# Kernel optimization log

Measured on AMD Instinct MI355X. Metric: run time of the kernel, lower is better.

The kernel has to match this reference:

```python
import jax, jax.numpy as jnp
import numpy as np

N = 50000
E = 600000
IN_DIM = 128
HID = 128
TIME_EMB = 32
T_STEPS = 100


def setup_inputs() -> dict:
    key = jax.random.key(0)
    ks = jax.random.split(key, 24)
    def lin_w(k, fi, fo):
        return (jax.random.normal(k, (fi, fo), jnp.float32) / np.sqrt(fi)).astype(jnp.float32)
    inp = {
        "target_features": jax.random.normal(ks[0], (N, IN_DIM), jnp.float32),
        "edge_index_v1": jax.random.randint(ks[1], (2, E), 0, N),
        "edge_index_v2": jax.random.randint(ks[2], (2, E), 0, N),
        "t": 57,
        "noise_v1": jax.random.normal(ks[3], (N, HID), jnp.float32),
        "noise_v2": jax.random.normal(ks[4], (N, HID), jnp.float32),
        # encoder GCN weights
        "enc_W1": lin_w(ks[5], IN_DIM, HID), "enc_b1": jnp.zeros((HID,), jnp.float32),
        "enc_W2": lin_w(ks[6], HID, HID),    "enc_b2": jnp.zeros((HID,), jnp.float32),
        # denoiser time MLP
        "tm_W1": lin_w(ks[7], 1, TIME_EMB),       "tm_b1": jnp.zeros((TIME_EMB,), jnp.float32),
        "tm_W2": lin_w(ks[8], TIME_EMB, HID),     "tm_b2": jnp.zeros((HID,), jnp.float32),
        # denoiser GCNs
        "g1_W": lin_w(ks[9], 3 * HID, HID), "g1_b": jnp.zeros((HID,), jnp.float32),
        "g2_W": lin_w(ks[10], HID, HID),    "g2_b": jnp.zeros((HID,), jnp.float32),
        "g3_W": lin_w(ks[11], HID, HID),    "g3_b": jnp.zeros((HID,), jnp.float32),
    }
    return inp


def _gcn_norm(edge_index, n):
    # add self-loops, symmetric normalization (PyG GCNConv default)
    loops = jnp.arange(n)
    src = jnp.concatenate([edge_index[0], loops])
    dst = jnp.concatenate([edge_index[1], loops])
    deg = jax.ops.segment_sum(jnp.ones_like(dst, dtype=jnp.float32), dst, num_segments=n)
    dinv = jnp.where(deg > 0, jax.lax.rsqrt(deg), 0.0)
    norm = dinv[src] * dinv[dst]  # (E+N,)
    return src, dst, norm


def _gcn(x, W, b, src, dst, norm, n):
    h = x @ W                                    # (N, out)
    msg = h[src] * norm[:, None]                 # gather + scale
    return jax.ops.segment_sum(msg, dst, num_segments=n) + b  # scatter-add


def reference(target_features, edge_index_v1, edge_index_v2, t, noise_v1, noise_v2,
              enc_W1, enc_b1, enc_W2, enc_b2,
              tm_W1, tm_b1, tm_W2, tm_b2,
              g1_W, g1_b, g2_W, g2_b, g3_W, g3_b):
    n = target_features.shape[0]
    e1 = _gcn_norm(edge_index_v1, n)
    e2 = _gcn_norm(edge_index_v2, n)

    def encoder(x, ed):
        h = jax.nn.relu(_gcn(x, enc_W1, enc_b1, *ed, n))
        return _gcn(h, enc_W2, enc_b2, *ed, n)

    h0_v1 = encoder(target_features, e1)
    h0_v2 = encoder(target_features, e2)

    # linear beta schedule coefficients at timestep t
    betas = jnp.linspace(1e-4, 0.02, T_STEPS)
    alpha_bars = jnp.cumprod(1.0 - betas)
    sqrt_ab = jnp.sqrt(alpha_bars)[t]
    sqrt_1m = jnp.sqrt(1.0 - alpha_bars)[t]

    h_t_v1 = sqrt_ab * h0_v1 + sqrt_1m * noise_v1
    h_t_v2 = sqrt_ab * h0_v2 + sqrt_1m * noise_v2

    # time embedding (same scalar t expanded to all nodes)
    t_float = jnp.full((n, 1), t, jnp.float32)
    t_emb = jax.nn.silu(t_float @ tm_W1 + tm_b1) @ tm_W2 + tm_b2  # (N, HID)

    def denoiser(h_self, h_other, ed):
        h = jnp.concatenate([h_self, h_other, t_emb], axis=-1)  # (N, 3*HID)
        h = jax.nn.relu(_gcn(h, g1_W, g1_b, *ed, n))
        h = jax.nn.relu(_gcn(h, g2_W, g2_b, *ed, n))
        return _gcn(h, g3_W, g3_b, *ed, n)

    pred_v1 = denoiser(h_t_v1, h_t_v2, e1)
    pred_v2 = denoiser(h_t_v2, h_t_v1, e2)

    L_diff = jnp.mean((pred_v1 - noise_v1) ** 2) + jnp.mean((pred_v2 - noise_v2) ** 2)
    h_diff = 0.5 * (h0_v1 + h0_v2)
    return h_diff, L_diff
```

## Files before the change

### kernel.cpp

```cpp
#include <hip/hip_runtime.h>

#define NN 50000
#define NE 600000

typedef __attribute__((ext_vector_type(8))) short short8;
typedef __attribute__((ext_vector_type(4))) float f32x4;

static inline int divup(int a, int b) { return (a + b - 1) / b; }

__device__ inline unsigned short f2bf(float f) {
    unsigned int u = __float_as_uint(f);
    unsigned int r = (u + 0x7FFFu + ((u >> 16) & 1u)) >> 16;
    return (unsigned short)r;
}
__device__ inline float bflo(unsigned int u) { return __uint_as_float(u << 16); }
__device__ inline float bfhi(unsigned int u) { return __uint_as_float(u & 0xFFFF0000u); }


__global__ void k_zero_int(int* p, int n) {
    int i = blockIdx.x * blockDim.x + threadIdx.x;
    int stride = gridDim.x * blockDim.x;
    for (; i < n; i += stride) p[i] = 0;
}

__global__ void k_scalars(const int* __restrict__ t_p,
                          const float* __restrict__ tmW1, const float* __restrict__ tmb1,
                          const float* __restrict__ tmW2, const float* __restrict__ tmb2,
                          const float* __restrict__ g1W,
                          float* __restrict__ scal, float* __restrict__ lout) {
    __shared__ float e32[32];
    __shared__ float temb[128];
    const int tid = threadIdx.x;
    const int t = t_p[0];
    if (tid < 32) {
        float x = (float)t * tmW1[tid] + tmb1[tid];
        e32[tid] = x / (1.0f + expf(-x));
    }
    __syncthreads();
    float acc = tmb2[tid];
    for (int j = 0; j < 32; ++j) acc += e32[j] * tmW2[j * 128 + tid];
    temb[tid] = acc;
    __syncthreads();
    float cv = 0.0f;
    for (int j = 0; j < 128; ++j) cv += temb[j] * g1W[(256 + j) * 128 + tid];
    scal[2 + tid] = cv;
    if (tid == 0) {
        double ab = 1.0;
        for (int i = 0; i <= t; ++i) {
            double beta = 1e-4 + (0.02 - 1e-4) * (double)i / 99.0;
            ab *= (1.0 - beta);
        }
        scal[0] = (float)sqrt(ab);
        scal[1] = (float)sqrt(1.0 - ab);
        lout[0] = 0.0f;
    }
}

__global__ void k_wprep(const float* __restrict__ encW1, const float* __restrict__ encW2,
                        const float* __restrict__ g1W, const float* __restrict__ g2W,
                        const float* __restrict__ g3W, unsigned short* __restrict__ WtS) {
    int i = blockIdx.x * blockDim.x + threadIdx.x;
    if (i >= 6 * 16384) return;
    int m = i >> 14;
    int r = i & 16383;
    int k = r >> 7;
    int n = r & 127;
    const float* src;
    switch (m) {
        case 0: src = encW1; break;
        case 1: src = encW2; break;
        case 2: src = g1W; break;
        case 3: src = g1W + 16384; break;
        case 4: src = g2W; break;
        default: src = g3W; break;
    }
    unsigned short v = f2bf(src[k * 128 + n]);
    unsigned int byte = (((unsigned)n << 8) | ((unsigned)k << 1)) ^ (((unsigned)n & 7u) << 4);
    WtS[(m << 14) + (byte >> 1)] = v;
}

__global__ void k_xcast(const float* __restrict__ in, unsigned short* __restrict__ out, int n4) {
    int i = blockIdx.x * blockDim.x + threadIdx.x;
    int stride = gridDim.x * blockDim.x;
    for (; i < n4; i += stride) {
        float4 v = ((const float4*)in)[i];
        ushort4 o;
        o.x = f2bf(v.x); o.y = f2bf(v.y); o.z = f2bf(v.z); o.w = f2bf(v.w);
        ((ushort4*)out)[i] = o;
    }
}

__global__ void k_hist(const int* __restrict__ dst, int* __restrict__ cnt, int e) {
    int i = blockIdx.x * blockDim.x + threadIdx.x;
    if (i < e) atomicAdd(&cnt[dst[i]], 1);
}

#define SCAN_B 256
__global__ void k_scan1(const int* __restrict__ cnt, int* __restrict__ exc,
                        int* __restrict__ bsum, int n) {
    __shared__ int s[SCAN_B];
    int i = blockIdx.x * SCAN_B + threadIdx.x;
    int v = (i < n) ? cnt[i] : 0;
    s[threadIdx.x] = v;
    __syncthreads();
    for (int off = 1; off < SCAN_B; off <<= 1) {
        int tv = (threadIdx.x >= off) ? s[threadIdx.x - off] : 0;
        __syncthreads();
        s[threadIdx.x] += tv;
        __syncthreads();
    }
    if (i < n) exc[i] = s[threadIdx.x] - v;
    if (threadIdx.x == SCAN_B - 1) bsum[blockIdx.x] = s[SCAN_B - 1];
}

__global__ void k_scan2(int* __restrict__ bsum, int nb) {
    __shared__ int s[SCAN_B];
    int v = (threadIdx.x < nb) ? bsum[threadIdx.x] : 0;
    s[threadIdx.x] = v;
    __syncthreads();
    for (int off = 1; off < SCAN_B; off <<= 1) {
        int tv = (threadIdx.x >= off) ? s[threadIdx.x - off] : 0;
        __syncthreads();
        s[threadIdx.x] += tv;
        __syncthreads();
    }
    if (threadIdx.x < nb) bsum[threadIdx.x] = s[threadIdx.x] - v;
}

__global__ void k_scan3(int* __restrict__ exc, const int* __restrict__ bsum, int n, int total) {
    int i = blockIdx.x * SCAN_B + threadIdx.x;
    if (i < n) exc[i] += bsum[blockIdx.x];
    if (i == 0) exc[n] = total;
}

__global__ void k_fill(const int* __restrict__ src, const int* __restrict__ dst,
                       const int* __restrict__ rowptr, int* __restrict__ fill,
                       int* __restrict__ colA, int e) {
    int i = blockIdx.x * blockDim.x + threadIdx.x;
    if (i < e) {
        int d = dst[i];
        int p = atomicAdd(&fill[d], 1);
        colA[rowptr[d] + p] = src[i];
    }
}

__global__ void k_dinv(const int* __restrict__ cnt, float* __restrict__ dinv, int n) {
    int i = blockIdx.x * blockDim.x + threadIdx.x;
    if (i < n) dinv[i] = rsqrtf((float)cnt[i] + 1.0f);
}

__global__ __launch_bounds__(256) void k_mgemm(
    const unsigned short* __restrict__ A, const unsigned short* __restrict__ Wa,
    const unsigned short* __restrict__ B, const unsigned short* __restrict__ Wb,
    const float* __restrict__ cvec, unsigned short* __restrict__ out, int nrows) {
    __shared__ unsigned short sW[16384];
    const int tid = threadIdx.x;
    const int wv = tid >> 6;
    const int l = tid & 63;
    const int lrow = l & 15;
    const int lk = l >> 4;
    const int r0 = blockIdx.x * 64 + wv * 16;

    f32x4 acc[8];
#pragma unroll
    for (int ct = 0; ct < 8; ++ct) acc[ct] = (f32x4){0.f, 0.f, 0.f, 0.f};

    const unsigned short* Aptr[2] = {A, B};
    const unsigned short* Wptr[2] = {Wa, Wb};
    const int np = (B != nullptr) ? 2 : 1;

    int arow = r0 + lrow;
    if (arow >= nrows) arow = nrows - 1;

    for (int p = 0; p < np; ++p) {
        __syncthreads();
        {
            const uint4* s = (const uint4*)Wptr[p];
            uint4* d = (uint4*)sW;
#pragma unroll
            for (int j = 0; j < 8; ++j) d[tid + j * 256] = s[tid + j * 256];
        }
        __syncthreads();
        const unsigned short* abase = Aptr[p] + (size_t)arow * 128 + lk * 8;
#pragma unroll
        for (int ks = 0; ks < 4; ++ks) {
            short8 af = *(const short8*)(abase + ks * 32);
            const int kb2 = (lk * 8 + ks * 32) << 1;
#pragma unroll
            for (int ct = 0; ct < 8; ++ct) {
                int n = ct * 16 + lrow;
                int byteoff = ((n << 8) + kb2) ^ ((l & 7) << 4);
                short8 bf = *(const short8*)((const char*)sW + byteoff);
                acc[ct] = __builtin_amdgcn_mfma_f32_16x16x32_bf16(af, bf, acc[ct], 0, 0, 0);
            }
        }
    }
#pragma unroll
    for (int ct = 0; ct < 8; ++ct) {
        float cv = cvec ? cvec[ct * 16 + lrow] : 0.0f;
#pragma unroll
        for (int rg = 0; rg < 4; ++rg) {
            int row = r0 + lk * 4 + rg;
            if (row < nrows) out[(size_t)row * 128 + ct * 16 + lrow] = f2bf(acc[ct][rg] + cv);
        }
    }
}

__global__ __launch_bounds__(256) void k_agg(
    const unsigned short* __restrict__ h, const int* __restrict__ rowptr,
    const int* __restrict__ colA, const float* __restrict__ dinv,
    const float* __restrict__ bias, unsigned short* __restrict__ out, int n, int do_relu) {
    const int d = (blockIdx.x * blockDim.x + threadIdx.x) >> 6;
    const int l = threadIdx.x & 63;
    if (d >= n) return;
    const int lg = l >> 4;
    const int ll = l & 15;
    const float di = dinv[d];

    float acc[8];
#pragma unroll
    for (int k = 0; k < 8; ++k) acc[k] = 0.0f;

    const int e0 = rowptr[d];
    const int e1 = rowptr[d + 1];
    for (int base = e0; base < e1; base += 64) {
        int cnt = min(64, e1 - base);
        int cs = 0;
        float ws = 0.0f;
        if (base + l < e1) {
            cs = colA[base + l];
            ws = dinv[cs];
        }
        for (int j4 = 0; j4 < cnt; j4 += 4) {
            int idx = j4 + lg;
            int s = __shfl(cs, idx);
            float w = __shfl(ws, idx);
            uint4 u = *((const uint4*)(h + (size_t)s * 128) + ll);
            acc[0] += w * bflo(u.x);
            acc[1] += w * bfhi(u.x);
            acc[2] += w * bflo(u.y);
            acc[3] += w * bfhi(u.y);
            acc[4] += w * bflo(u.z);
            acc[5] += w * bfhi(u.z);
            acc[6] += w * bflo(u.w);
            acc[7] += w * bfhi(u.w);
        }
    }
#pragma unroll
    for (int k = 0; k < 8; ++k) {
        acc[k] += __shfl_xor(acc[k], 16);
        acc[k] += __shfl_xor(acc[k], 32);
    }
    if (lg == 0) {
        uint4 su = *((const uint4*)(h + (size_t)d * 128) + ll);
        float4 b0 = ((const float4*)bias)[ll * 2];
        float4 b1 = ((const float4*)bias)[ll * 2 + 1];
        float sf[8] = {bflo(su.x), bfhi(su.x), bflo(su.y), bfhi(su.y),
                       bflo(su.z), bfhi(su.z), bflo(su.w), bfhi(su.w)};
        float bb[8] = {b0.x, b0.y, b0.z, b0.w, b1.x, b1.y, b1.z, b1.w};
        unsigned short o[8];
#pragma unroll
        for (int k = 0; k < 8; ++k) {
            float v = di * (acc[k] + di * sf[k]) + bb[k];
            if (do_relu) v = fmaxf(v, 0.0f);
            o[k] = f2bf(v);
        }
        uint4 ov;
        ov.x = (unsigned int)o[0] | ((unsigned int)o[1] << 16);
        ov.y = (unsigned int)o[2] | ((unsigned int)o[3] << 16);
        ov.z = (unsigned int)o[4] | ((unsigned int)o[5] << 16);
        ov.w = (unsigned int)o[6] | ((unsigned int)o[7] << 16);
        *((uint4*)(out + (size_t)d * 128) + ll) = ov;
    }
}

__global__ void k_mix(const unsigned short* __restrict__ F1, const unsigned short* __restrict__ F2,
                      const float* __restrict__ n1, const float* __restrict__ n2,
                      const float* __restrict__ scal, float* __restrict__ hdiff,
                      unsigned short* __restrict__ B1, unsigned short* __restrict__ B2, int total2) {
    const float sa = scal[0];
    const float sm = scal[1];
    int i = blockIdx.x * blockDim.x + threadIdx.x;
    const int stride = gridDim.x * blockDim.x;
    for (; i < total2; i += stride) {
        unsigned int u1 = ((const unsigned int*)F1)[i];
        unsigned int u2 = ((const unsigned int*)F2)[i];
        float a0 = bflo(u1), a1 = bfhi(u1);
        float b0 = bflo(u2), b1 = bfhi(u2);
        float2 x = ((const float2*)n1)[i];
        float2 y = ((const float2*)n2)[i];
        float2 hd;
        hd.x = 0.5f * (a0 + b0);
        hd.y = 0.5f * (a1 + b1);
        ((float2*)hdiff)[i] = hd;
        float h1x = sa * a0 + sm * x.x, h1y = sa * a1 + sm * x.y;
        float h2x = sa * b0 + sm * y.x, h2y = sa * b1 + sm * y.y;
        ((unsigned int*)B1)[i] = (unsigned int)f2bf(h1x) | ((unsigned int)f2bf(h1y) << 16);
        ((unsigned int*)B2)[i] = (unsigned int)f2bf(h2x) | ((unsigned int)f2bf(h2y) << 16);
    }
}

__global__ void k_loss(const unsigned short* __restrict__ P1, const unsigned short* __restrict__ P2,
                       const float* __restrict__ n1, const float* __restrict__ n2,
                       float* __restrict__ outs, int total2, float inv_total) {
    float s = 0.0f;
    int i = blockIdx.x * blockDim.x + threadIdx.x;
    const int stride = gridDim.x * blockDim.x;
    for (; i < total2; i += stride) {
        unsigned int u1 = ((const unsigned int*)P1)[i];
        unsigned int u2 = ((const unsigned int*)P2)[i];
        float2 x = ((const float2*)n1)[i];
        float2 y = ((const float2*)n2)[i];
        float d0 = bflo(u1) - x.x, d1 = bfhi(u1) - x.y;
        float d2 = bflo(u2) - y.x, d3 = bfhi(u2) - y.y;
        s += d0 * d0 + d1 * d1 + d2 * d2 + d3 * d3;
    }
    __shared__ float red[4];
    for (int off = 32; off > 0; off >>= 1) s += __shfl_down(s, off, 64);
    const int lane = threadIdx.x & 63;
    const int wid = threadIdx.x >> 6;
    if (lane == 0) red[wid] = s;
    __syncthreads();
    if (threadIdx.x == 0) {
        float t = red[0] + red[1] + red[2] + red[3];
        atomicAdd(outs, t * inv_total);
    }
}

extern "C" void kernel_launch(void* const* d_in, const int* in_sizes, int n_in,
                              void* d_out, int out_size, void* d_ws, size_t ws_size,
                              hipStream_t stream) {
    const float* X      = (const float*)d_in[0];
    const int*   ei1    = (const int*)d_in[1];
    const int*   ei2    = (const int*)d_in[2];
    const int*   t_p    = (const int*)d_in[3];
    const float* noise1 = (const float*)d_in[4];
    const float* noise2 = (const float*)d_in[5];
    const float* encW1  = (const float*)d_in[6];
    const float* encb1  = (const float*)d_in[7];
    const float* encW2  = (const float*)d_in[8];
    const float* encb2  = (const float*)d_in[9];
    const float* tmW1   = (const float*)d_in[10];
    const float* tmb1   = (const float*)d_in[11];
    const float* tmW2   = (const float*)d_in[12];
    const float* tmb2   = (const float*)d_in[13];
    const float* g1W    = (const float*)d_in[14];
    const float* g1b    = (const float*)d_in[15];
    const float* g2W    = (const float*)d_in[16];
    const float* g2b    = (const float*)d_in[17];
    const float* g3W    = (const float*)d_in[18];
    const float* g3b    = (const float*)d_in[19];

    float* out_hdiff = (float*)d_out;
    float* out_L     = (float*)d_out + (size_t)NN * 128;

    char* p = (char*)d_ws;
    auto alloc = [&](size_t bytes) -> void* {
        void* r = (void*)p;
        p += (bytes + 255) & ~(size_t)255;
        return r;
    };
    int* cnts = (int*)alloc((size_t)4 * NN * sizeof(int));
    int *cnt1 = cnts, *cnt2 = cnts + NN, *fill1 = cnts + 2 * NN, *fill2 = cnts + 3 * NN;
    int* rowptr1 = (int*)alloc((NN + 1) * sizeof(int));
    int* rowptr2 = (int*)alloc((NN + 1) * sizeof(int));
    int* bsum    = (int*)alloc(256 * sizeof(int));
    int* col1    = (int*)alloc((size_t)NE * sizeof(int));
    int* col2    = (int*)alloc((size_t)NE * sizeof(int));
    float* dinv1 = (float*)alloc(NN * sizeof(float));
    float* dinv2 = (float*)alloc(NN * sizeof(float));
    float* scal  = (float*)alloc(256 * sizeof(float));
    unsigned short* WtS = (unsigned short*)alloc((size_t)6 * 16384 * sizeof(unsigned short));
    const size_t FB = (size_t)NN * 128;
    unsigned short* Xb = (unsigned short*)alloc(FB * 2);
    unsigned short* A1 = (unsigned short*)alloc(FB * 2);
    unsigned short* A2 = (unsigned short*)alloc(FB * 2);
    unsigned short* D0 = (unsigned short*)alloc(FB * 2);
    unsigned short* F1 = (unsigned short*)alloc(FB * 2);
    unsigned short* F2 = (unsigned short*)alloc(FB * 2);
    unsigned short* V1d = Xb;
    unsigned short* V2d = F2;

    const unsigned short* W_enc1 = WtS;
    const unsigned short* W_enc2 = WtS + 1 * 16384;
    const unsigned short* W_g1a  = WtS + 2 * 16384;
    const unsigned short* W_g1b  = WtS + 3 * 16384;
    const unsigned short* W_g2   = WtS + 4 * 16384;
    const unsigned short* W_g3   = WtS + 5 * 16384;

    const int* src1 = ei1;
    const int* dst1 = ei1 + NE;
    const int* src2 = ei2;
    const int* dst2 = ei2 + NE;

    const int nbN   = divup(NN, 256);
    const int nbE   = divup(NE, 256);
    const int nb4N  = divup(4 * NN, 256);
    const int nbG   = divup(NN, 64);
    const int nbAgg = divup(NN, 4);
    const int total2 = NN * 64;

    k_zero_int<<<nb4N, 256, 0, stream>>>(cnts, 4 * NN);
    k_scalars<<<1, 128, 0, stream>>>(t_p, tmW1, tmb1, tmW2, tmb2, g1W, scal, out_L);
    k_wprep<<<divup(6 * 16384, 256), 256, 0, stream>>>(encW1, encW2, g1W, g2W, g3W, WtS);
    k_xcast<<<2048, 256, 0, stream>>>(X, Xb, NN * 32);
    k_hist<<<nbE, 256, 0, stream>>>(dst1, cnt1, NE);
    k_hist<<<nbE, 256, 0, stream>>>(dst2, cnt2, NE);
    k_scan1<<<nbN, 256, 0, stream>>>(cnt1, rowptr1, bsum, NN);
    k_scan2<<<1, 256, 0, stream>>>(bsum, nbN);
    k_scan3<<<nbN, 256, 0, stream>>>(rowptr1, bsum, NN, NE);
    k_scan1<<<nbN, 256, 0, stream>>>(cnt2, rowptr2, bsum, NN);
    k_scan2<<<1, 256, 0, stream>>>(bsum, nbN);
    k_scan3<<<nbN, 256, 0, stream>>>(rowptr2, bsum, NN, NE);
    k_dinv<<<nbN, 256, 0, stream>>>(cnt1, dinv1, NN);
    k_dinv<<<nbN, 256, 0, stream>>>(cnt2, dinv2, NN);
    k_fill<<<nbE, 256, 0, stream>>>(src1, dst1, rowptr1, fill1, col1, NE);
    k_fill<<<nbE, 256, 0, stream>>>(src2, dst2, rowptr2, fill2, col2, NE);

    k_mgemm<<<nbG, 256, 0, stream>>>(Xb, W_enc1, nullptr, nullptr, nullptr, D0, NN);
    k_agg<<<nbAgg, 256, 0, stream>>>(D0, rowptr1, col1, dinv1, encb1, A1, NN, 1);
    k_agg<<<nbAgg, 256, 0, stream>>>(D0, rowptr2, col2, dinv2, encb1, A2, NN, 1);
    k_mgemm<<<nbG, 256, 0, stream>>>(A1, W_enc2, nullptr, nullptr, nullptr, D0, NN);
    k_agg<<<nbAgg, 256, 0, stream>>>(D0, rowptr1, col1, dinv1, encb2, F1, NN, 0);
    k_mgemm<<<nbG, 256, 0, stream>>>(A2, W_enc2, nullptr, nullptr, nullptr, D0, NN);
    k_agg<<<nbAgg, 256, 0, stream>>>(D0, rowptr2, col2, dinv2, encb2, F2, NN, 0);

    k_mix<<<2048, 256, 0, stream>>>(F1, F2, noise1, noise2, scal, out_hdiff, A1, A2, total2);

    k_mgemm<<<nbG, 256, 0, stream>>>(A1, W_g1a, A2, W_g1b, scal + 2, D0, NN);
    k_agg<<<nbAgg, 256, 0, stream>>>(D0, rowptr1, col1, dinv1, g1b, V1d, NN, 1);
    k_mgemm<<<nbG, 256, 0, stream>>>(A2, W_g1a, A1, W_g1b, scal + 2, D0, NN);
    k_agg<<<nbAgg, 256, 0, stream>>>(D0, rowptr2, col2, dinv2, g1b, V2d, NN, 1);

    k_mgemm<<<nbG, 256, 0, stream>>>(V1d, W_g2, nullptr, nullptr, nullptr, D0, NN);
    k_agg<<<nbAgg, 256, 0, stream>>>(D0, rowptr1, col1, dinv1, g2b, V1d, NN, 1);
    k_mgemm<<<nbG, 256, 0, stream>>>(V2d, W_g2, nullptr, nullptr, nullptr, D0, NN);
    k_agg<<<nbAgg, 256, 0, stream>>>(D0, rowptr2, col2, dinv2, g2b, V2d, NN, 1);

    k_mgemm<<<nbG, 256, 0, stream>>>(V1d, W_g3, nullptr, nullptr, nullptr, D0, NN);
    k_agg<<<nbAgg, 256, 0, stream>>>(D0, rowptr1, col1, dinv1, g3b, F1, NN, 0);
    k_mgemm<<<nbG, 256, 0, stream>>>(V2d, W_g3, nullptr, nullptr, nullptr, D0, NN);
    k_agg<<<nbAgg, 256, 0, stream>>>(D0, rowptr2, col2, dinv2, g3b, F2, NN, 0);

    k_loss<<<2048, 256, 0, stream>>>(F1, F2, noise1, noise2, out_L, total2,
                                     1.0f / (float)((size_t)NN * 128));
}
```

Measured before the change: 787.4 us.

## Batch both graph views into shared launches and prefetch neighbor rows in aggregation

Merges the zeroing, input cast and weight prep into one kernel, and fuses the two histogram, scan, dinv and fill passes across both views. Prefix sums now run in a single 1024-thread block. Each GEMM and aggregation launch handles both views at once, which cuts about 30 launches to about 13 and fills the GPU better. The aggregation loop loads the next neighbor row before accumulating the current one, and a second D buffer is added. The single-block scan over 100k counts is serial per thread and could become a bottleneck.

```diff
diff --git a/kernel.cpp b/kernel.cpp
--- a/kernel.cpp
+++ b/kernel.cpp
@@ -2,6 +2,7 @@
 
 #define NN 50000
 #define NE 600000
+#define NBG 782
 
 typedef __attribute__((ext_vector_type(8))) short short8;
 typedef __attribute__((ext_vector_type(4))) float f32x4;
@@ -16,11 +17,47 @@
 __device__ inline float bflo(unsigned int u) { return __uint_as_float(u << 16); }
 __device__ inline float bfhi(unsigned int u) { return __uint_as_float(u & 0xFFFF0000u); }
 
-
-__global__ void k_zero_int(int* p, int n) {
+#define PREP_Z (4 * NN)
+#define PREP_X (NN * 32)
+#define PREP_W (6 * 16384)
+__global__ void k_prep(const float* __restrict__ X,
+                       const float* __restrict__ encW1, const float* __restrict__ encW2,
+                       const float* __restrict__ g1W, const float* __restrict__ g2W,
+                       const float* __restrict__ g3W,
+                       int* __restrict__ cnts, unsigned short* __restrict__ Xb,
+                       unsigned short* __restrict__ WtS) {
     int i = blockIdx.x * blockDim.x + threadIdx.x;
-    int stride = gridDim.x * blockDim.x;
-    for (; i < n; i += stride) p[i] = 0;
+    const int stride = gridDim.x * blockDim.x;
+    const int T = PREP_Z + PREP_X + PREP_W;
+    for (; i < T; i += stride) {
+        if (i < PREP_Z) {
+            cnts[i] = 0;
+        } else if (i < PREP_Z + PREP_X) {
+            int j = i - PREP_Z;
+            float4 v = ((const float4*)X)[j];
+            ushort4 o;
+            o.x = f2bf(v.x); o.y = f2bf(v.y); o.z = f2bf(v.z); o.w = f2bf(v.w);
+            ((ushort4*)Xb)[j] = o;
+        } else {
+            int j = i - (PREP_Z + PREP_X);
+            int m = j >> 14;
+            int r = j & 16383;
+            int k = r >> 7;
+            int n = r & 127;
+            const float* src;
+            switch (m) {
+                case 0: src = encW1; break;
+                case 1: src = encW2; break;
+                case 2: src = g1W; break;
+                case 3: src = g1W + 16384; break;
+                case 4: src = g2W; break;
+                default: src = g3W; break;
+            }
+            unsigned short v = f2bf(src[k * 128 + n]);
+            unsigned int byte = (((unsigned)n << 8) | ((unsigned)k << 1)) ^ (((unsigned)n & 7u) << 4);
+            WtS[(m << 14) + (byte >> 1)] = v;
+        }
+    }
 }
 
 __global__ void k_scalars(const int* __restrict__ t_p,
@@ -56,110 +93,85 @@
     }
 }
 
-__global__ void k_wprep(const float* __restrict__ encW1, const float* __restrict__ encW2,
-                        const float* __restrict__ g1W, const float* __restrict__ g2W,
-                        const float* __restrict__ g3W, unsigned short* __restrict__ WtS) {
+__global__ void k_hist2(const int* __restrict__ dst1, const int* __restrict__ dst2,
+                        int* __restrict__ cnt1, int* __restrict__ cnt2) {
     int i = blockIdx.x * blockDim.x + threadIdx.x;
-    if (i >= 6 * 16384) return;
-    int m = i >> 14;
-    int r = i & 16383;
-    int k = r >> 7;
-    int n = r & 127;
-    const float* src;
-    switch (m) {
-        case 0: src = encW1; break;
-        case 1: src = encW2; break;
-        case 2: src = g1W; break;
-        case 3: src = g1W + 16384; break;
-        case 4: src = g2W; break;
-        default: src = g3W; break;
-    }
-    unsigned short v = f2bf(src[k * 128 + n]);
-    unsigned int byte = (((unsigned)n << 8) | ((unsigned)k << 1)) ^ (((unsigned)n & 7u) << 4);
-    WtS[(m << 14) + (byte >> 1)] = v;
-}
-
-__global__ void k_xcast(const float* __restrict__ in, unsigned short* __restrict__ out, int n4) {
+    if (i < NE) atomicAdd(&cnt1[dst1[i]], 1);
+    else if (i < 2 * NE) atomicAdd(&cnt2[dst2[i - NE]], 1);
+}
+
+__global__ __launch_bounds__(1024) void k_scanfull(
+    const int* __restrict__ cnt, int* __restrict__ rowptr1, int* __restrict__ rowptr2,
+    float* __restrict__ dinv1, float* __restrict__ dinv2) {
+    __shared__ int part[1024];
+    const int tid = threadIdx.x;
+    const int total = 2 * NN;
+    const int per = (total + 1023) >> 10;
+    int s0 = tid * per; if (s0 > total) s0 = total;
+    int s1 = s0 + per; if (s1 > total) s1 = total;
+    int sum = 0;
+    for (int i = s0; i < s1; ++i) sum += cnt[i];
+    part[tid] = sum;
+    __syncthreads();
+    for (int off = 1; off < 1024; off <<= 1) {
+        int v = (tid >= off) ? part[tid - off] : 0;
+        __syncthreads();
+        part[tid] += v;
+        __syncthreads();
+    }
+    int run = part[tid] - sum;
+    for (int i = s0; i < s1; ++i) {
+        int c = cnt[i];
+        if (i < NN) {
+            rowptr1[i] = run;
+            dinv1[i] = rsqrtf((float)c + 1.0f);
+        } else {
+            rowptr2[i - NN] = run - NE;
+            dinv2[i - NN] = rsqrtf((float)c + 1.0f);
+        }
+        run += c;
+    }
+    if (tid == 0) { rowptr1[NN] = NE; rowptr2[NN] = NE; }
+}
+
+__global__ void k_fill2(const int* __restrict__ src1, const int* __restrict__ dst1,
+                        const int* __restrict__ src2, const int* __restrict__ dst2,
+                        const int* __restrict__ rowptr1, const int* __restrict__ rowptr2,
+                        int* __restrict__ fill1, int* __restrict__ fill2,
+                        int* __restrict__ col1, int* __restrict__ col2) {
     int i = blockIdx.x * blockDim.x + threadIdx.x;
-    int stride = gridDim.x * blockDim.x;
-    for (; i < n4; i += stride) {
-        float4 v = ((const float4*)in)[i];
-        ushort4 o;
-        o.x = f2bf(v.x); o.y = f2bf(v.y); o.z = f2bf(v.z); o.w = f2bf(v.w);
-        ((ushort4*)out)[i] = o;
-    }
-}
-
-__global__ void k_hist(const int* __restrict__ dst, int* __restrict__ cnt, int e) {
-    int i = blockIdx.x * blockDim.x + threadIdx.x;
-    if (i < e) atomicAdd(&cnt[dst[i]], 1);
-}
-
-#define SCAN_B 256
-__global__ void k_scan1(const int* __restrict__ cnt, int* __restrict__ exc,
-                        int* __restrict__ bsum, int n) {
-    __shared__ int s[SCAN_B];
-    int i = blockIdx.x * SCAN_B + threadIdx.x;
-    int v = (i < n) ? cnt[i] : 0;
-    s[threadIdx.x] = v;
-    __syncthreads();
-    for (int off = 1; off < SCAN_B; off <<= 1) {
-        int tv = (threadIdx.x >= off) ? s[threadIdx.x - off] : 0;
-        __syncthreads();
-        s[threadIdx.x] += tv;
-        __syncthreads();
-    }
-    if (i < n) exc[i] = s[threadIdx.x] - v;
-    if (threadIdx.x == SCAN_B - 1) bsum[blockIdx.x] = s[SCAN_B - 1];
-}
-
-__global__ void k_scan2(int* __restrict__ bsum, int nb) {
-    __shared__ int s[SCAN_B];
-    int v = (threadIdx.x < nb) ? bsum[threadIdx.x] : 0;
-    s[threadIdx.x] = v;
-    __syncthreads();
-    for (int off = 1; off < SCAN_B; off <<= 1) {
-        int tv = (threadIdx.x >= off) ? s[threadIdx.x - off] : 0;
-        __syncthreads();
-        s[threadIdx.x] += tv;
-        __syncthreads();
-    }
-    if (threadIdx.x < nb) bsum[threadIdx.x] = s[threadIdx.x] - v;
-}
-
-__global__ void k_scan3(int* __restrict__ exc, const int* __restrict__ bsum, int n, int total) {
-    int i = blockIdx.x * SCAN_B + threadIdx.x;
-    if (i < n) exc[i] += bsum[blockIdx.x];
-    if (i == 0) exc[n] = total;
-}
-
-__global__ void k_fill(const int* __restrict__ src, const int* __restrict__ dst,
-                       const int* __restrict__ rowptr, int* __restrict__ fill,
-                       int* __restrict__ colA, int e) {
-    int i = blockIdx.x * blockDim.x + threadIdx.x;
-    if (i < e) {
-        int d = dst[i];
-        int p = atomicAdd(&fill[d], 1);
-        colA[rowptr[d] + p] = src[i];
-    }
-}
-
-__global__ void k_dinv(const int* __restrict__ cnt, float* __restrict__ dinv, int n) {
-    int i = blockIdx.x * blockDim.x + threadIdx.x;
-    if (i < n) dinv[i] = rsqrtf((float)cnt[i] + 1.0f);
-}
-
-__global__ __launch_bounds__(256) void k_mgemm(
-    const unsigned short* __restrict__ A, const unsigned short* __restrict__ Wa,
-    const unsigned short* __restrict__ B, const unsigned short* __restrict__ Wb,
-    const float* __restrict__ cvec, unsigned short* __restrict__ out, int nrows) {
+    if (i < NE) {
+        int d = dst1[i];
+        int p = atomicAdd(&fill1[d], 1);
+        col1[rowptr1[d] + p] = src1[i];
+    } else if (i < 2 * NE) {
+        int j = i - NE;
+        int d = dst2[j];
+        int p = atomicAdd(&fill2[d], 1);
+        col2[rowptr2[d] + p] = src2[j];
+    }
+}
+
+__global__ __launch_bounds__(256) void k_mgemm2(
+    const unsigned short* __restrict__ A0, const unsigned short* __restrict__ B0,
+    unsigned short* __restrict__ out0,
+    const unsigned short* __restrict__ A1, const unsigned short* __restrict__ B1,
+    unsigned short* __restrict__ out1,
+    const unsigned short* __restrict__ Wa, const unsigned short* __restrict__ Wb,
+    const float* __restrict__ cvec) {
     __shared__ unsigned short sW[16384];
+    const int unit = blockIdx.x / NBG;
+    const int blk = blockIdx.x - unit * NBG;
+    const unsigned short* A = unit ? A1 : A0;
+    const unsigned short* B = unit ? B1 : B0;
+    unsigned short* out = unit ? out1 : out0;
+
     const int tid = threadIdx.x;
     const int wv = tid >> 6;
     const int l = tid & 63;
     const int lrow = l & 15;
     const int lk = l >> 4;
-    const int r0 = blockIdx.x * 64 + wv * 16;
+    const int r0 = blk * 64 + wv * 16;
 
     f32x4 acc[8];
 #pragma unroll
@@ -170,7 +182,7 @@
     const int np = (B != nullptr) ? 2 : 1;
 
     int arow = r0 + lrow;
-    if (arow >= nrows) arow = nrows - 1;
+    if (arow >= NN) arow = NN - 1;
 
     for (int p = 0; p < np; ++p) {
         __syncthreads();
@@ -201,18 +213,28 @@
 #pragma unroll
         for (int rg = 0; rg < 4; ++rg) {
             int row = r0 + lk * 4 + rg;
-            if (row < nrows) out[(size_t)row * 128 + ct * 16 + lrow] = f2bf(acc[ct][rg] + cv);
-        }
-    }
-}
-
-__global__ __launch_bounds__(256) void k_agg(
-    const unsigned short* __restrict__ h, const int* __restrict__ rowptr,
-    const int* __restrict__ colA, const float* __restrict__ dinv,
-    const float* __restrict__ bias, unsigned short* __restrict__ out, int n, int do_relu) {
-    const int d = (blockIdx.x * blockDim.x + threadIdx.x) >> 6;
+            if (row < NN) out[(size_t)row * 128 + ct * 16 + lrow] = f2bf(acc[ct][rg] + cv);
+        }
+    }
+}
+
+__global__ __launch_bounds__(256) void k_agg2(
+    const unsigned short* __restrict__ in0, const unsigned short* __restrict__ in1,
+    const int* __restrict__ rowptr1, const int* __restrict__ col1, const float* __restrict__ dinv1,
+    const int* __restrict__ rowptr2, const int* __restrict__ col2, const float* __restrict__ dinv2,
+    const float* __restrict__ bias,
+    unsigned short* __restrict__ out0, unsigned short* __restrict__ out1, int do_relu) {
+    const int gw = (blockIdx.x * blockDim.x + threadIdx.x) >> 6;
+    if (gw >= 2 * NN) return;
+    const int unit = gw >= NN;
+    const int d = unit ? gw - NN : gw;
+    const unsigned short* h = unit ? in1 : in0;
+    const int* rowptr = unit ? rowptr2 : rowptr1;
+    const int* colA = unit ? col2 : col1;
+    const float* dinv = unit ? dinv2 : dinv1;
+    unsigned short* out = unit ? out1 : out0;
+
     const int l = threadIdx.x & 63;
-    if (d >= n) return;
     const int lg = l >> 4;
     const int ll = l & 15;
     const float di = dinv[d];
@@ -231,20 +253,32 @@
             cs = colA[base + l];
             ws = dinv[cs];
         }
-        for (int j4 = 0; j4 < cnt; j4 += 4) {
-            int idx = j4 + lg;
-            int s = __shfl(cs, idx);
-            float w = __shfl(ws, idx);
-            uint4 u = *((const uint4*)(h + (size_t)s * 128) + ll);
-            acc[0] += w * bflo(u.x);
-            acc[1] += w * bfhi(u.x);
-            acc[2] += w * bflo(u.y);
-            acc[3] += w * bfhi(u.y);
-            acc[4] += w * bflo(u.z);
-            acc[5] += w * bfhi(u.z);
-            acc[6] += w * bflo(u.w);
-            acc[7] += w * bfhi(u.w);
-        }
+        int s0 = __shfl(cs, lg);
+        float w0 = __shfl(ws, lg);
+        uint4 u0 = *((const uint4*)(h + (size_t)s0 * 128) + ll);
+        for (int j4 = 4; j4 < cnt; j4 += 4) {
+            int s1 = __shfl(cs, j4 + lg);
+            float w1 = __shfl(ws, j4 + lg);
+            uint4 u1 = *((const uint4*)(h + (size_t)s1 * 128) + ll);
+            acc[0] += w0 * bflo(u0.x);
+            acc[1] += w0 * bfhi(u0.x);
+            acc[2] += w0 * bflo(u0.y);
+            acc[3] += w0 * bfhi(u0.y);
+            acc[4] += w0 * bflo(u0.z);
+            acc[5] += w0 * bfhi(u0.z);
+            acc[6] += w0 * bflo(u0.w);
+            acc[7] += w0 * bfhi(u0.w);
+            u0 = u1;
+            w0 = w1;
+        }
+        acc[0] += w0 * bflo(u0.x);
+        acc[1] += w0 * bfhi(u0.x);
+        acc[2] += w0 * bflo(u0.y);
+        acc[3] += w0 * bfhi(u0.y);
+        acc[4] += w0 * bflo(u0.z);
+        acc[5] += w0 * bfhi(u0.z);
+        acc[6] += w0 * bflo(u0.w);
+        acc[7] += w0 * bfhi(u0.w);
     }
 #pragma unroll
     for (int k = 0; k < 8; ++k) {
@@ -364,7 +398,6 @@
     int *cnt1 = cnts, *cnt2 = cnts + NN, *fill1 = cnts + 2 * NN, *fill2 = cnts + 3 * NN;
     int* rowptr1 = (int*)alloc((NN + 1) * sizeof(int));
     int* rowptr2 = (int*)alloc((NN + 1) * sizeof(int));
-    int* bsum    = (int*)alloc(256 * sizeof(int));
     int* col1    = (int*)alloc((size_t)NE * sizeof(int));
     int* col2    = (int*)alloc((size_t)NE * sizeof(int));
     float* dinv1 = (float*)alloc(NN * sizeof(float));
@@ -376,6 +409,7 @@
     unsigned short* A1 = (unsigned short*)alloc(FB * 2);
     unsigned short* A2 = (unsigned short*)alloc(FB * 2);
     unsigned short* D0 = (unsigned short*)alloc(FB * 2);
+    unsigned short* D1 = (unsigned short*)alloc(FB * 2);
     unsigned short* F1 = (unsigned short*)alloc(FB * 2);
     unsigned short* F2 = (unsigned short*)alloc(FB * 2);
     unsigned short* V1d = Xb;
@@ -393,54 +427,39 @@
     const int* src2 = ei2;
     const int* dst2 = ei2 + NE;
 
-    const int nbN   = divup(NN, 256);
-    const int nbE   = divup(NE, 256);
-    const int nb4N  = divup(4 * NN, 256);
-    const int nbG   = divup(NN, 64);
-    const int nbAgg = divup(NN, 4);
+    const int nbE2  = divup(2 * NE, 256);
+    const int nbAgg = divup(2 * NN, 4);
     const int total2 = NN * 64;
 
-    k_zero_int<<<nb4N, 256, 0, stream>>>(cnts, 4 * NN);
+    k_prep<<<2048, 256, 0, stream>>>(X, encW1, encW2, g1W, g2W, g3W, cnts, Xb, WtS);
     k_scalars<<<1, 128, 0, stream>>>(t_p, tmW1, tmb1, tmW2, tmb2, g1W, scal, out_L);
-    k_wprep<<<divup(6 * 16384, 256), 256, 0, stream>>>(encW1, encW2, g1W, g2W, g3W, WtS);
-    k_xcast<<<2048, 256, 0, stream>>>(X, Xb, NN * 32);
-    k_hist<<<nbE, 256, 0, stream>>>(dst1, cnt1, NE);
-    k_hist<<<nbE, 256, 0, stream>>>(dst2, cnt2, NE);
-    k_scan1<<<nbN, 256, 0, stream>>>(cnt1, rowptr1, bsum, NN);
-    k_scan2<<<1, 256, 0, stream>>>(bsum, nbN);
-    k_scan3<<<nbN, 256, 0, stream>>>(rowptr1, bsum, NN, NE);
-    k_scan1<<<nbN, 256, 0, stream>>>(cnt2, rowptr2, bsum, NN);
-    k_scan2<<<1, 256, 0, stream>>>(bsum, nbN);
-    k_scan3<<<nbN, 256, 0, stream>>>(rowptr2, bsum, NN, NE);
-    k_dinv<<<nbN, 256, 0, stream>>>(cnt1, dinv1, NN);
-    k_dinv<<<nbN, 256, 0, stream>>>(cnt2, dinv2, NN);
-    k_fill<<<nbE, 256, 0, stream>>>(src1, dst1, rowptr1, fill1, col1, NE);
-    k_fill<<<nbE, 256, 0, stream>>>(src2, dst2, rowptr2, fill2, col2, NE);
-
-    k_mgemm<<<nbG, 256, 0, stream>>>(Xb, W_enc1, nullptr, nullptr, nullptr, D0, NN);
-    k_agg<<<nbAgg, 256, 0, stream>>>(D0, rowptr1, col1, dinv1, encb1, A1, NN, 1);
-    k_agg<<<nbAgg, 256, 0, stream>>>(D0, rowptr2, col2, dinv2, encb1, A2, NN, 1);
-    k_mgemm<<<nbG, 256, 0, stream>>>(A1, W_enc2, nullptr, nullptr, nullptr, D0, NN);
-    k_agg<<<nbAgg, 256, 0, stream>>>(D0, rowptr1, col1, dinv1, encb2, F1, NN, 0);
-    k_mgemm<<<nbG, 256, 0, stream>>>(A2, W_enc2, nullptr, nullptr, nullptr, D0, NN);
-    k_agg<<<nbAgg, 256, 0, stream>>>(D0, rowptr2, col2, dinv2, encb2, F2, NN, 0);
+    k_hist2<<<nbE2, 256, 0, stream>>>(dst1, dst2, cnt1, cnt2);
+    k_scanfull<<<1, 1024, 0, stream>>>(cnts, rowptr1, rowptr2, dinv1, dinv2);
+    k_fill2<<<nbE2, 256, 0, stream>>>(src1, dst1, src2, dst2, rowptr1, rowptr2,
+                                      fill1, fill2, col1, col2);
+
+    k_mgemm2<<<NBG, 256, 0, stream>>>(Xb, nullptr, D0, nullptr, nullptr, nullptr,
+                                      W_enc1, nullptr, nullptr);
+    k_agg2<<<nbAgg, 256, 0, stream>>>(D0, D0, rowptr1, col1, dinv1, rowptr2, col2, dinv2,
+                                      encb1, A1, A2, 1);
+    k_mgemm2<<<2 * NBG, 256, 0, stream>>>(A1, nullptr, D0, A2, nullptr, D1,
+                                          W_enc2, nullptr, nullptr);
+    k_agg2<<<nbAgg, 256, 0, stream>>>(D0, D1, rowptr1, col1, dinv1, rowptr2, col2, dinv2,
+                                      encb2, F1, F2, 0);
 
     k_mix<<<2048, 256, 0, stream>>>(F1, F2, noise1, noise2, scal, out_hdiff, A1, A2, total2);
 
-    k_mgemm<<<nbG, 256, 0, stream>>>(A1, W_g1a, A2, W_g1b, scal + 2, D0, NN);
-    k_agg<<<nbAgg, 256, 0, stream>>>(D0, rowptr1, col1, dinv1, g1b, V1d, NN, 1);
-    k_mgemm<<<nbG, 256, 0, stream>>>(A2, W_g1a, A1, W_g1b, scal + 2, D0, NN);
-    k_agg<<<nbAgg, 256, 0, stream>>>(D0, rowptr2, col2, dinv2, g1b, V2d, NN, 1);
-
-    k_mgemm<<<nbG, 256, 0, stream>>>(V1d, W_g2, nullptr, nullptr, nullptr, D0, NN);
-    k_agg<<<nbAgg, 256, 0, stream>>>(D0, rowptr1, col1, dinv1, g2b, V1d, NN, 1);
-    k_mgemm<<<nbG, 256, 0, stream>>>(V2d, W_g2, nullptr, nullptr, nullptr, D0, NN);
-    k_agg<<<nbAgg, 256, 0, stream>>>(D0, rowptr2, col2, dinv2, g2b, V2d, NN, 1);
-
-    k_mgemm<<<nbG, 256, 0, stream>>>(V1d, W_g3, nullptr, nullptr, nullptr, D0, NN);
-    k_agg<<<nbAgg, 256, 0, stream>>>(D0, rowptr1, col1, dinv1, g3b, F1, NN, 0);
-    k_mgemm<<<nbG, 256, 0, stream>>>(V2d, W_g3, nullptr, nullptr, nullptr, D0, NN);
-    k_agg<<<nbAgg, 256, 0, stream>>>(D0, rowptr2, col2, dinv2, g3b, F2, NN, 0);
+    k_mgemm2<<<2 * NBG, 256, 0, stream>>>(A1, A2, D0, A2, A1, D1, W_g1a, W_g1b, scal + 2);
+    k_agg2<<<nbAgg, 256, 0, stream>>>(D0, D1, rowptr1, col1, dinv1, rowptr2, col2, dinv2,
+                                      g1b, V1d, V2d, 1);
+    k_mgemm2<<<2 * NBG, 256, 0, stream>>>(V1d, nullptr, D0, V2d, nullptr, D1,
+                                          W_g2, nullptr, nullptr);
+    k_agg2<<<nbAgg, 256, 0, stream>>>(D0, D1, rowptr1, col1, dinv1, rowptr2, col2, dinv2,
+                                      g2b, V1d, V2d, 1);
+    k_mgemm2<<<2 * NBG, 256, 0, stream>>>(V1d, nullptr, D0, V2d, nullptr, D1,
+                                          W_g3, nullptr, nullptr);
+    k_agg2<<<nbAgg, 256, 0, stream>>>(D0, D1, rowptr1, col1, dinv1, rowptr2, col2, dinv2,
+                                      g3b, F1, F2, 0);
 
     k_loss<<<2048, 256, 0, stream>>>(F1, F2, noise1, noise2, out_L, total2,
                                      1.0f / (float)((size_t)NN * 128));
```

Result: slower. 906.3 us (+15.1%).
